# Kernel tuning notes

Hardware: AMD Instinct MI355X
Metric: run time of the kernel (lower is better)

## Reference

```python
import jax, jax.numpy as jnp
import numpy as np

N = 500000        # total atoms (n1 nodes)
G = 20000         # graphs (g nodes)
D_IN = 128        # in_features
D_H = 256         # hidden width (config_local / mid_features)
D_OUT = 1         # final output per graph (config_global last int)


def setup_inputs() -> dict:
    key = jax.random.key(0)
    ks = jax.random.split(key, 10)
    h = jax.random.normal(ks[0], (N, D_IN), dtype=jnp.float32)
    graph_ids = jnp.sort(jax.random.randint(ks[1], (N,), 0, G))
    s = 0.05
    return {
        "h": h,
        "graph_ids": graph_ids,
        "num_graphs": G,
        # d_local: Linear(128->256) relu, Linear(256->256) relu
        "W1": jax.random.normal(ks[2], (D_IN, D_H), dtype=jnp.float32) * s,
        "b1": jnp.zeros((D_H,), dtype=jnp.float32),
        "W2": jax.random.normal(ks[3], (D_H, D_H), dtype=jnp.float32) * s,
        "b2": jnp.zeros((D_H,), dtype=jnp.float32),
        # d_global: Linear(256->256) relu, Linear(256->1)
        "Wg1": jax.random.normal(ks[4], (D_H, D_H), dtype=jnp.float32) * s,
        "bg1": jnp.zeros((D_H,), dtype=jnp.float32),
        "Wg2": jax.random.normal(ks[5], (D_H, D_OUT), dtype=jnp.float32) * s,
        "bg2": jnp.zeros((D_OUT,), dtype=jnp.float32),
    }


def reference(h, graph_ids, num_graphs, W1, b1, W2, b2, Wg1, bg1, Wg2, bg2):
    # node-level MLP (d_local): h_global per n1 node
    x = jax.nn.relu(h @ W1 + b1)            # [N, D_H]
    x = jax.nn.relu(x @ W2 + b2)            # [N, D_H]
    # copy_src + sum over n1_in_g edges == per-graph segment sum
    pooled = jax.ops.segment_sum(x, graph_ids, num_segments=num_graphs)  # [G, D_H]
    # graph-level MLP (d_global)
    y = jax.nn.relu(pooled @ Wg1 + bg1)     # [G, D_H]
    return y @ Wg2 + bg2                    # [G, 1]
```

## Files before the change

### kernel.cpp

```cpp
#include <hip/hip_runtime.h>
#include <stdint.h>

#define D_IN 128
#define D_H  256
#define BMN  32
#define BMG  64

typedef float f32x4 __attribute__((ext_vector_type(4)));
typedef short s16x8 __attribute__((ext_vector_type(8)));
typedef unsigned int u32x2 __attribute__((ext_vector_type(2)));
typedef unsigned int u32x4 __attribute__((ext_vector_type(4)));

__device__ __forceinline__ unsigned short f2bf(float x) {
  union { float f; uint32_t u; } v; v.f = x;
  uint32_t r = v.u + 0x7fffu + ((v.u >> 16) & 1u);
  return (unsigned short)(r >> 16);
}
__device__ __forceinline__ float bf2f(unsigned short u) {
  union { uint32_t u; float f; } v; v.u = (uint32_t)u << 16;
  return v.f;
}
__device__ __forceinline__ uint32_t pkbf(float lo, float hi) {
#if __has_builtin(__builtin_amdgcn_cvt_pk_bf16_f32)
  auto r = __builtin_amdgcn_cvt_pk_bf16_f32(lo, hi);
  uint32_t u; __builtin_memcpy(&u, &r, 4); return u;
#else
  return (uint32_t)f2bf(lo) | ((uint32_t)f2bf(hi) << 16);
#endif
}

__global__ void prep_kernel(const float* __restrict__ W1, const float* __restrict__ W2,
                            const float* __restrict__ Wg1,
                            float* __restrict__ pooled, unsigned short* __restrict__ W1t,
                            unsigned short* __restrict__ W2t, unsigned short* __restrict__ Wg1t,
                            int pooled_n) {
  int stride = gridDim.x * blockDim.x;
  int tid = blockIdx.x * blockDim.x + threadIdx.x;
  float4 z4 = make_float4(0.f, 0.f, 0.f, 0.f);
  for (int i = tid; i < (pooled_n >> 2); i += stride) ((float4*)pooled)[i] = z4;
  for (int i = tid; i < D_H * D_IN; i += stride) {
    int n = i >> 7, k = i & (D_IN - 1);
    W1t[i] = f2bf(W1[k * D_H + n]);
  }
  for (int i = tid; i < D_H * D_H; i += stride) {
    int n = i >> 8, k = i & (D_H - 1);
    W2t[i]  = f2bf(W2[k * D_H + n]);
    Wg1t[i] = f2bf(Wg1[k * D_H + n]);
  }
}

__global__ __launch_bounds__(256, 5)
void node_kernel(const float* __restrict__ h, const int* __restrict__ gids,
                 const float* __restrict__ b1, const float* __restrict__ b2,
                 const unsigned short* __restrict__ W1t, const unsigned short* __restrict__ W2t,
                 float* __restrict__ pooled, int nnodes) {
  __shared__ unsigned short buf[BMN * D_H];
  __shared__ int sgid[BMN];
  const int tid  = threadIdx.x;
  const int lane = tid & 63;
  const int wave = tid >> 6;
  const int lr   = lane & 15;
  const int q    = lane >> 4;
  const int row0 = blockIdx.x * BMN;
  unsigned short* hA = buf + 4096;

  const unsigned short* w1base = W1t + (wave * 64 + lr) * D_IN + q * 8;
  const unsigned short* w2base = W2t + (wave * 64 + lr) * D_H + q * 8;

  s16x8 a[2][4];
  #pragma unroll
  for (int mt = 0; mt < 4; ++mt) a[0][mt] = *(const s16x8*)(w1base + mt * 16 * D_IN + 0 * 32);
  #pragma unroll
  for (int mt = 0; mt < 4; ++mt) a[1][mt] = *(const s16x8*)(w1base + mt * 16 * D_IN + 1 * 32);

  if (tid < BMN) {
    int gr = row0 + tid;
    sgid[tid] = (gr < nnodes) ? gids[gr] : -1;
  }

  #pragma unroll
  for (int i = 0; i < 2; ++i) {
    int gi = tid + i * 256, r = gi >> 4, gc = gi & 15, gr = row0 + r;
    f32x4 v0 = (f32x4){0.f, 0.f, 0.f, 0.f}, v1 = v0;
    if (gr < nnodes) {
      const f32x4* p = (const f32x4*)(h + (size_t)gr * D_IN + gc * 8);
      v0 = __builtin_nontemporal_load(p);
      v1 = __builtin_nontemporal_load(p + 1);
    }
    u32x4 u;
    u[0] = pkbf(v0[0], v0[1]); u[1] = pkbf(v0[2], v0[3]);
    u[2] = pkbf(v1[0], v1[1]); u[3] = pkbf(v1[2], v1[3]);
    *(u32x4*)&hA[r * D_IN + ((gc ^ (r & 7)) << 3)] = u;
  }
  __syncthreads();

  f32x4 acc[4][2];
  #pragma unroll
  for (int mt = 0; mt < 4; ++mt)
    #pragma unroll
    for (int nt = 0; nt < 2; ++nt)
      acc[mt][nt] = (f32x4){0.f, 0.f, 0.f, 0.f};

  #pragma unroll
  for (int ks = 0; ks < 4; ++ks) {
    const int kq = ks * 32 + q * 8;
    s16x8 b[2];
    #pragma unroll
    for (int nt = 0; nt < 2; ++nt)
      b[nt] = *(const s16x8*)&hA[(nt * 16 + lr) * D_IN + (((kq >> 3) ^ (lr & 7)) << 3)];
    #pragma unroll
    for (int mt = 0; mt < 4; ++mt)
      #pragma unroll
      for (int nt = 0; nt < 2; ++nt)
        acc[mt][nt] = __builtin_amdgcn_mfma_f32_16x16x32_bf16(a[ks & 1][mt], b[nt], acc[mt][nt], 0, 0, 0);
    if (ks < 2) {
      #pragma unroll
      for (int mt = 0; mt < 4; ++mt)
        a[ks & 1][mt] = *(const s16x8*)(w1base + mt * 16 * D_IN + (ks + 2) * 32);
    } else {
      #pragma unroll
      for (int mt = 0; mt < 4; ++mt)
        a[ks & 1][mt] = *(const s16x8*)(w2base + mt * 16 * D_H + (ks - 2) * 32);
    }
  }

  __syncthreads();

  #pragma unroll
  for (int mt = 0; mt < 4; ++mt) {
    int f = wave * 64 + mt * 16 + q * 4;
    float4 bias = *(const float4*)&b1[f];
    #pragma unroll
    for (int nt = 0; nt < 2; ++nt) {
      int nd = nt * 16 + lr;
      u32x2 w;
      w[0] = pkbf(fmaxf(acc[mt][nt][0] + bias.x, 0.f), fmaxf(acc[mt][nt][1] + bias.y, 0.f));
      w[1] = pkbf(fmaxf(acc[mt][nt][2] + bias.z, 0.f), fmaxf(acc[mt][nt][3] + bias.w, 0.f));
      *(u32x2*)&buf[nd * D_H + (((f >> 3) ^ (nd & 7)) << 3) + (f & 7)] = w;
    }
  }
  __syncthreads();

  #pragma unroll
  for (int mt = 0; mt < 4; ++mt)
    #pragma unroll
    for (int nt = 0; nt < 2; ++nt)
      acc[mt][nt] = (f32x4){0.f, 0.f, 0.f, 0.f};

  #pragma unroll
  for (int ks = 0; ks < 8; ++ks) {
    const int kq = ks * 32 + q * 8;
    s16x8 b[2];
    #pragma unroll
    for (int nt = 0; nt < 2; ++nt)
      b[nt] = *(const s16x8*)&buf[(nt * 16 + lr) * D_H + (((kq >> 3) ^ (lr & 7)) << 3)];
    #pragma unroll
    for (int mt = 0; mt < 4; ++mt)
      #pragma unroll
      for (int nt = 0; nt < 2; ++nt)
        acc[mt][nt] = __builtin_amdgcn_mfma_f32_16x16x32_bf16(a[ks & 1][mt], b[nt], acc[mt][nt], 0, 0, 0);
    if (ks < 6) {
      #pragma unroll
      for (int mt = 0; mt < 4; ++mt)
        a[ks & 1][mt] = *(const s16x8*)(w2base + mt * 16 * D_H + (ks + 2) * 32);
    }
  }
  __syncthreads();

  #pragma unroll
  for (int mt = 0; mt < 4; ++mt) {
    int f = wave * 64 + mt * 16 + q * 4;
    float4 bias = *(const float4*)&b2[f];
    #pragma unroll
    for (int nt = 0; nt < 2; ++nt) {
      int nd = nt * 16 + lr;
      u32x2 w;
      w[0] = pkbf(fmaxf(acc[mt][nt][0] + bias.x, 0.f), fmaxf(acc[mt][nt][1] + bias.y, 0.f));
      w[1] = pkbf(fmaxf(acc[mt][nt][2] + bias.z, 0.f), fmaxf(acc[mt][nt][3] + bias.w, 0.f));
      *(u32x2*)&buf[nd * D_H + (((f >> 3) ^ (nd & 7)) << 3) + (f & 7)] = w;
    }
  }

  {
    const int hi = tid >> 3, lo = tid & 7;
    float racc = 0.f;
    for (int r = 0; r < BMN; ++r) {
      int g = sgid[r];
      if (g >= 0) {
        racc += bf2f(buf[r * D_H + ((hi ^ (r & 7)) << 3) + lo]);
        if (r == BMN - 1 || sgid[r + 1] != g) {
          atomicAdd(&pooled[g * D_H + tid], racc);
          racc = 0.f;
        }
      }
    }
  }
}

__global__ __launch_bounds__(256, 4)
void graph_kernel(const float* __restrict__ pooled, const float* __restrict__ bg1,
                  const unsigned short* __restrict__ Wg1t, const float* __restrict__ Wg2,
                  const float* __restrict__ bg2, float* __restrict__ out, int ngraphs) {
  __shared__ unsigned short pA[BMG * D_H];
  const int tid  = threadIdx.x;
  const int lane = tid & 63;
  const int wave = tid >> 6;
  const int lr   = lane & 15;
  const int q    = lane >> 4;
  const int g0   = blockIdx.x * BMG;

  #pragma unroll
  for (int i = 0; i < 8; ++i) {
    int gi = tid + i * 256, r = gi >> 5, gc = gi & 31;
    int gr = g0 + r;
    f32x4 v0 = (f32x4){0.f, 0.f, 0.f, 0.f}, v1 = v0;
    if (gr < ngraphs) {
      const f32x4* p = (const f32x4*)(pooled + (size_t)gr * D_H + gc * 8);
      v0 = p[0]; v1 = p[1];
    }
    u32x4 u;
    u[0] = pkbf(v0[0], v0[1]); u[1] = pkbf(v0[2], v0[3]);
    u[2] = pkbf(v1[0], v1[1]); u[3] = pkbf(v1[2], v1[3]);
    *(u32x4*)&pA[r * D_H + (((gc & 7) ^ (r & 7)) << 3) + ((gc & 24) << 3)] = u;
  }
  __syncthreads();

  f32x4 acc[4][4];
  #pragma unroll
  for (int mt = 0; mt < 4; ++mt)
    #pragma unroll
    for (int nt = 0; nt < 4; ++nt)
      acc[mt][nt] = (f32x4){0.f, 0.f, 0.f, 0.f};

  #pragma unroll
  for (int ks = 0; ks < 8; ++ks) {
    const int kq = ks * 32 + q * 8;
    s16x8 a[4], b[4];
    #pragma unroll
    for (int mt = 0; mt < 4; ++mt)
      a[mt] = *(const s16x8*)&Wg1t[(wave * 64 + mt * 16 + lr) * D_H + kq];
    #pragma unroll
    for (int nt = 0; nt < 4; ++nt) {
      int row = nt * 16 + lr, gw = kq >> 3;
      b[nt] = *(const s16x8*)&pA[row * D_H + (((gw & 7) ^ (row & 7)) << 3) + ((gw & 24) << 3)];
    }
    #pragma unroll
    for (int mt = 0; mt < 4; ++mt)
      #pragma unroll
      for (int nt = 0; nt < 4; ++nt)
        acc[mt][nt] = __builtin_amdgcn_mfma_f32_16x16x32_bf16(a[mt], b[nt], acc[mt][nt], 0, 0, 0);
  }
  __syncthreads();

  #pragma unroll
  for (int mt = 0; mt < 4; ++mt) {
    int f = wave * 64 + mt * 16 + q * 4;
    float4 bias = *(const float4*)&bg1[f];
    #pragma unroll
    for (int nt = 0; nt < 4; ++nt) {
      int nd = nt * 16 + lr;
      u32x2 w;
      w[0] = pkbf(fmaxf(acc[mt][nt][0] + bias.x, 0.f), fmaxf(acc[mt][nt][1] + bias.y, 0.f));
      w[1] = pkbf(fmaxf(acc[mt][nt][2] + bias.z, 0.f), fmaxf(acc[mt][nt][3] + bias.w, 0.f));
      int gw = f >> 3;
      *(u32x2*)&pA[nd * D_H + (((gw & 7) ^ (nd & 7)) << 3) + ((gw & 24) << 3) + (f & 7)] = w;
    }
  }
  __syncthreads();

  int gloc = tid >> 2;
  int part = tid & 3;
  float p = 0.f;
  #pragma unroll 8
  for (int i = 0; i < 32; ++i) {
    int f2 = part + 4 * i;
    int hw = 2 * f2;
    int gw = hw >> 3;
    uint32_t wv = *(const uint32_t*)&pA[gloc * D_H + (((gw & 7) ^ (gloc & 7)) << 3) +
                                        ((gw & 24) << 3) + (hw & 7)];
    float2 wg = ((const float2*)Wg2)[f2];
    p += bf2f((unsigned short)(wv & 0xffffu)) * wg.x +
         bf2f((unsigned short)(wv >> 16)) * wg.y;
  }
  p += __shfl_xor(p, 1);
  p += __shfl_xor(p, 2);
  if (part == 0 && (g0 + gloc) < ngraphs)
    out[g0 + gloc] = p + bg2[0];
}

extern "C" void kernel_launch(void* const* d_in, const int* in_sizes, int n_in,
                              void* d_out, int out_size, void* d_ws, size_t ws_size,
                              hipStream_t stream) {
  const float* h   = (const float*)d_in[0];
  const int*   gid = (const int*)d_in[1];
  const float* W1  = (const float*)d_in[3];
  const float* b1  = (const float*)d_in[4];
  const float* W2  = (const float*)d_in[5];
  const float* b2  = (const float*)d_in[6];
  const float* Wg1 = (const float*)d_in[7];
  const float* bg1 = (const float*)d_in[8];
  const float* Wg2 = (const float*)d_in[9];
  const float* bg2 = (const float*)d_in[10];
  float* out = (float*)d_out;

  const int N = in_sizes[1];
  const int G = out_size;

  char* ws = (char*)d_ws;
  float* pooled = (float*)ws;
  size_t off = (size_t)G * D_H * sizeof(float);
  unsigned short* W1t  = (unsigned short*)(ws + off); off += (size_t)D_H * D_IN * 2;
  unsigned short* W2t  = (unsigned short*)(ws + off); off += (size_t)D_H * D_H * 2;
  unsigned short* Wg1t = (unsigned short*)(ws + off);

  prep_kernel<<<512, 256, 0, stream>>>(W1, W2, Wg1, pooled, W1t, W2t, Wg1t, G * D_H);
  node_kernel<<<(N + BMN - 1) / BMN, 256, 0, stream>>>(h, gid, b1, b2, W1t, W2t, pooled, N);
  graph_kernel<<<(G + BMG - 1) / BMG, 256, 0, stream>>>(pooled, bg1, Wg1t, Wg2, bg2, out, G);
}
```

Baseline: 675.2 us.

## Double node tile to 64 rows and split segment-sum across row groups

The node kernel now processes 64 nodes per block instead of 32, doubling the MFMA N-tiles per wave so each weight fragment loaded from global memory is reused across twice as many rows. The pooling step is restructured so each thread handles four features across a 16-row quarter of the tile, reading them as one vector LDS load. The goal is to cut per-node weight traffic and the serial reduction loop length. In exchange it raises register and LDS use (occupancy bound drops from 5 to 4) and may issue more atomics, since each row quarter flushes partial sums separately.

```diff
diff --git a/kernel.cpp b/kernel.cpp
--- a/kernel.cpp
+++ b/kernel.cpp
@@ -3,7 +3,7 @@
 
 #define D_IN 128
 #define D_H  256
-#define BMN  32
+#define BM   64
 #define BMG  64
 
 typedef float f32x4 __attribute__((ext_vector_type(4)));
@@ -49,20 +49,20 @@
   }
 }
 
-__global__ __launch_bounds__(256, 5)
+__global__ __launch_bounds__(256, 4)
 void node_kernel(const float* __restrict__ h, const int* __restrict__ gids,
                  const float* __restrict__ b1, const float* __restrict__ b2,
                  const unsigned short* __restrict__ W1t, const unsigned short* __restrict__ W2t,
                  float* __restrict__ pooled, int nnodes) {
-  __shared__ unsigned short buf[BMN * D_H];
-  __shared__ int sgid[BMN];
+  __shared__ unsigned short buf[BM * D_H];
+  __shared__ int sgid[BM];
   const int tid  = threadIdx.x;
   const int lane = tid & 63;
   const int wave = tid >> 6;
   const int lr   = lane & 15;
   const int q    = lane >> 4;
-  const int row0 = blockIdx.x * BMN;
-  unsigned short* hA = buf + 4096;
+  const int row0 = blockIdx.x * BM;
+  unsigned short* hA = buf + 8192;
 
   const unsigned short* w1base = W1t + (wave * 64 + lr) * D_IN + q * 8;
   const unsigned short* w2base = W2t + (wave * 64 + lr) * D_H + q * 8;
@@ -73,13 +73,13 @@
   #pragma unroll
   for (int mt = 0; mt < 4; ++mt) a[1][mt] = *(const s16x8*)(w1base + mt * 16 * D_IN + 1 * 32);
 
-  if (tid < BMN) {
+  if (tid < BM) {
     int gr = row0 + tid;
     sgid[tid] = (gr < nnodes) ? gids[gr] : -1;
   }
 
   #pragma unroll
-  for (int i = 0; i < 2; ++i) {
+  for (int i = 0; i < 4; ++i) {
     int gi = tid + i * 256, r = gi >> 4, gc = gi & 15, gr = row0 + r;
     f32x4 v0 = (f32x4){0.f, 0.f, 0.f, 0.f}, v1 = v0;
     if (gr < nnodes) {
@@ -94,24 +94,24 @@
   }
   __syncthreads();
 
-  f32x4 acc[4][2];
+  f32x4 acc[4][4];
   #pragma unroll
   for (int mt = 0; mt < 4; ++mt)
     #pragma unroll
-    for (int nt = 0; nt < 2; ++nt)
+    for (int nt = 0; nt < 4; ++nt)
       acc[mt][nt] = (f32x4){0.f, 0.f, 0.f, 0.f};
 
   #pragma unroll
   for (int ks = 0; ks < 4; ++ks) {
     const int kq = ks * 32 + q * 8;
-    s16x8 b[2];
-    #pragma unroll
-    for (int nt = 0; nt < 2; ++nt)
+    s16x8 b[4];
+    #pragma unroll
+    for (int nt = 0; nt < 4; ++nt)
       b[nt] = *(const s16x8*)&hA[(nt * 16 + lr) * D_IN + (((kq >> 3) ^ (lr & 7)) << 3)];
     #pragma unroll
     for (int mt = 0; mt < 4; ++mt)
       #pragma unroll
-      for (int nt = 0; nt < 2; ++nt)
+      for (int nt = 0; nt < 4; ++nt)
         acc[mt][nt] = __builtin_amdgcn_mfma_f32_16x16x32_bf16(a[ks & 1][mt], b[nt], acc[mt][nt], 0, 0, 0);
     if (ks < 2) {
       #pragma unroll
@@ -131,7 +131,7 @@
     int f = wave * 64 + mt * 16 + q * 4;
     float4 bias = *(const float4*)&b1[f];
     #pragma unroll
-    for (int nt = 0; nt < 2; ++nt) {
+    for (int nt = 0; nt < 4; ++nt) {
       int nd = nt * 16 + lr;
       u32x2 w;
       w[0] = pkbf(fmaxf(acc[mt][nt][0] + bias.x, 0.f), fmaxf(acc[mt][nt][1] + bias.y, 0.f));
@@ -144,20 +144,20 @@
   #pragma unroll
   for (int mt = 0; mt < 4; ++mt)
     #pragma unroll
-    for (int nt = 0; nt < 2; ++nt)
+    for (int nt = 0; nt < 4; ++nt)
       acc[mt][nt] = (f32x4){0.f, 0.f, 0.f, 0.f};
 
   #pragma unroll
   for (int ks = 0; ks < 8; ++ks) {
     const int kq = ks * 32 + q * 8;
-    s16x8 b[2];
-    #pragma unroll
-    for (int nt = 0; nt < 2; ++nt)
+    s16x8 b[4];
+    #pragma unroll
+    for (int nt = 0; nt < 4; ++nt)
       b[nt] = *(const s16x8*)&buf[(nt * 16 + lr) * D_H + (((kq >> 3) ^ (lr & 7)) << 3)];
     #pragma unroll
     for (int mt = 0; mt < 4; ++mt)
       #pragma unroll
-      for (int nt = 0; nt < 2; ++nt)
+      for (int nt = 0; nt < 4; ++nt)
         acc[mt][nt] = __builtin_amdgcn_mfma_f32_16x16x32_bf16(a[ks & 1][mt], b[nt], acc[mt][nt], 0, 0, 0);
     if (ks < 6) {
       #pragma unroll
@@ -172,7 +172,7 @@
     int f = wave * 64 + mt * 16 + q * 4;
     float4 bias = *(const float4*)&b2[f];
     #pragma unroll
-    for (int nt = 0; nt < 2; ++nt) {
+    for (int nt = 0; nt < 4; ++nt) {
       int nd = nt * 16 + lr;
       u32x2 w;
       w[0] = pkbf(fmaxf(acc[mt][nt][0] + bias.x, 0.f), fmaxf(acc[mt][nt][1] + bias.y, 0.f));
@@ -182,15 +182,27 @@
   }
 
   {
-    const int hi = tid >> 3, lo = tid & 7;
-    float racc = 0.f;
-    for (int r = 0; r < BMN; ++r) {
+    const int f0  = wave * 64 + (lane & 15) * 4;
+    const int rg  = lane >> 4;
+    const int swz = f0 >> 3;
+    const int sub = f0 & 7;
+    float ra0 = 0.f, ra1 = 0.f, ra2 = 0.f, ra3 = 0.f;
+    for (int rr = 0; rr < 16; ++rr) {
+      int r = rg * 16 + rr;
       int g = sgid[r];
       if (g >= 0) {
-        racc += bf2f(buf[r * D_H + ((hi ^ (r & 7)) << 3) + lo]);
-        if (r == BMN - 1 || sgid[r + 1] != g) {
-          atomicAdd(&pooled[g * D_H + tid], racc);
-          racc = 0.f;
+        u32x2 wv = *(const u32x2*)&buf[r * D_H + ((swz ^ (r & 7)) << 3) + sub];
+        ra0 += bf2f((unsigned short)(wv[0] & 0xffffu));
+        ra1 += bf2f((unsigned short)(wv[0] >> 16));
+        ra2 += bf2f((unsigned short)(wv[1] & 0xffffu));
+        ra3 += bf2f((unsigned short)(wv[1] >> 16));
+        if (rr == 15 || sgid[r + 1] != g) {
+          float* dst = &pooled[g * D_H + f0];
+          atomicAdd(dst + 0, ra0);
+          atomicAdd(dst + 1, ra1);
+          atomicAdd(dst + 2, ra2);
+          atomicAdd(dst + 3, ra3);
+          ra0 = ra1 = ra2 = ra3 = 0.f;
         }
       }
     }
@@ -314,6 +326,6 @@
   unsigned short* Wg1t = (unsigned short*)(ws + off);
 
   prep_kernel<<<512, 256, 0, stream>>>(W1, W2, Wg1, pooled, W1t, W2t, Wg1t, G * D_H);
-  node_kernel<<<(N + BMN - 1) / BMN, 256, 0, stream>>>(h, gid, b1, b2, W1t, W2t, pooled, N);
+  node_kernel<<<(N + BM - 1) / BM, 256, 0, stream>>>(h, gid, b1, b2, W1t, W2t, pooled, N);
   graph_kernel<<<(G + BMG - 1) / BMG, 256, 0, stream>>>(pooled, bg1, Wg1t, Wg2, bg2, out, G);
 }
```

After: 633.8 us. 6.1% less time.
